# Kernel optimization log

Measured on AMD Instinct MI355X. Metric: run time of the kernel, lower is better.

Reference implementation:

```python
import jax, jax.numpy as jnp
import numpy as np
from jax import lax

C_LIGHT = 3e8
SPATIAL, CROP = 64, 128
BIN_LEN, WALL, SAMP_COEFF, CYCLES = 0.01, 2.0, 2.0, 5
B, D = 2, 1


def _waveconvparam(bin_resolution, virtual_wavelength, cycles):
    samples = int(round(cycles * virtual_wavelength / (C_LIGHT * bin_resolution)))
    num_cycles = samples * (C_LIGHT * bin_resolution) / virtual_wavelength
    sigma = 0.3
    g = np.arange(samples, dtype=np.float64)
    env = np.exp(-(((g - samples / 2.0) / (samples / 2.0)) ** 2) / (2 * sigma ** 2))
    cos_k = np.cos(2 * np.pi * num_cycles * g / samples) * env
    sin_k = np.sin(2 * np.pi * num_cycles * g / samples) * env
    return cos_k, sin_k


def _define_psf(N, M, slope):
    # LCT psf: locus of min |(4 slope)^2 (x^2+y^2) - z|, normalized and circularly shifted
    x = np.arange(2 * N, dtype=np.float64) / (2 * N - 1) * 2 - 1
    z = np.arange(2 * M, dtype=np.float64) / (2 * M - 1) * 2
    gy, gx, gz = np.meshgrid(x, x, z)  # (2N,2N,2M)
    blur = np.abs((4 * slope) ** 2 * (gx ** 2 + gy ** 2) - gz)
    d = (np.abs(blur - blur.min(axis=2, keepdims=True)) < 1e-8).astype(np.float64)
    e = d / np.sqrt(d.sum())
    f = np.roll(np.roll(e, N, axis=0), N, axis=1)
    return np.transpose(f, (2, 0, 1))  # (2M,2N,2N)


def _resampling_operator(M):
    row = M * M
    x = np.arange(1, row + 1, dtype=np.float64)
    mtx = np.zeros((row, M), dtype=np.float64)
    mtx[np.arange(row), np.ceil(np.sqrt(x)).astype(np.int64) - 1] = 1.0
    mtx = mtx / np.sqrt(x)[:, None]
    mtxi = mtx.T.copy()
    for _ in range(int(np.log2(M))):
        mtx = 0.5 * (mtx[0::2] + mtx[1::2])
        mtxi = 0.5 * (mtxi[:, 0::2] + mtxi[:, 1::2])
    return mtx.astype(np.float32), mtxi.astype(np.float32)


def setup_inputs() -> dict:
    key = jax.random.key(0)
    kf, kw, kb = jax.random.split(key, 3)
    bin_res = BIN_LEN / C_LIGHT
    trange = CROP * C_LIGHT * bin_res
    slope = (WALL / 2.0) / trange
    vlam = SAMP_COEFF * 2.0 * (WALL / (SPATIAL - 1))
    cos_k, sin_k = _waveconvparam(bin_res, vlam, CYCLES)
    wave = np.stack([cos_k, sin_k], 0)[:, ::-1][:, None, :].astype(np.float32)  # (2,1,k)
    psf = _define_psf(SPATIAL, CROP, slope)
    invpsf = np.conj(np.fft.fftn(psf))
    mtx, mtxi = _resampling_operator(CROP)
    return {
        "feature": jax.random.normal(kf, (B, D, CROP, SPATIAL, SPATIAL), jnp.float32),
        "conv_w": jax.random.normal(kw, ()) * 0.1 + 1.0,
        "conv_b": jax.random.normal(kb, ()) * 0.1,
        "wave": jnp.asarray(wave),
        "invpsf_real": jnp.asarray(np.real(invpsf).astype(np.float32))[None],
        "invpsf_imag": jnp.asarray(np.imag(invpsf).astype(np.float32))[None],
        "mtx": jnp.asarray(mtx),
        "mtxi": jnp.asarray(mtxi),
    }


def _attention(k1, k2, w, b):
    # SE-style cross attention; Conv3d(1,1,1) on unbatched (C=1,T,H,W) is w*x+b
    T = k2.shape[1]
    pe = jnp.sin(jnp.arange(T, dtype=k2.dtype))  # PE3D with 1 channel -> sin along T
    k2p = k2 + pe[None, :, None, None]
    scal = jnp.mean(w * k1 + b)  # conv + adaptive_avg_pool3d(1), channel dim = 1
    q = (w * k2p + b).reshape(1, 1, -1)
    attn = jax.nn.sigmoid(jax.nn.softmax(scal * q, axis=2)).reshape(k2p.shape)
    return attn * k2p


def _fre_atten2(kernel, w, b):
    _, T, H, W = kernel.shape
    ct, ch, cw = T // 2, H // 2, W // 2
    st, sh, sw = (T - ct) // 2, (H - ch) // 2, (W - cw) // 2
    sl = (slice(None), slice(ct - st, ct + st), slice(ch - sh, ch + sh), slice(cw - sw, cw + sw))
    high = kernel[sl]
    low = jnp.roll(kernel, (ct, ch, cw), axis=(1, 2, 3))[sl]
    l2l = _attention(low, low, w, b)
    l2h = _attention(l2l, high, w, b)
    temp = kernel.at[sl].set(l2h)
    temp = jnp.roll(temp, (ct, ch, cw), axis=(1, 2, 3)).at[sl].set(l2l)
    return jnp.roll(temp, (ct, ch, cw), axis=(1, 2, 3))


def _forward(feature, conv_w, conv_b, wave, invpsf_real, invpsf_imag, mtx, mtxi):
    b, d, T, H, W = feature.shape
    BD = b * d
    k = wave.shape[2]
    # virtual wave conv along time: (BDHW,1,T) x (2,1,k)
    data = feature.reshape(BD, T, H, W).transpose(0, 2, 3, 1).reshape(-1, 1, T)
    conv = lax.conv_general_dilated(data, wave, (1,), [(k // 2, k // 2)],
                                    dimension_numbers=("NCH", "OIH", "NCH"))
    if k % 2 == 0:
        conv = conv[:, :, 1:]
    data2 = conv.reshape(BD, H, W, 2, T).transpose(3, 0, 4, 1, 2).reshape(2 * BD, T, H, W)
    # temporal resampling then zero-pad to 2T,2H,2W
    tmp = jnp.einsum("tm,bmx->btx", mtx, data2.reshape(2 * BD, T, H * W)).reshape(2 * BD, T, H, W)
    datapad = jnp.zeros((2 * BD, 2 * T, 2 * H, 2 * W), feature.dtype).at[:, :T, :H, :W].set(tmp)
    datafre = jnp.fft.fftn(datapad)  # torch.fft.fftn transforms ALL dims incl. batch
    w1 = _fre_atten2(invpsf_real, conv_w, conv_b)
    w2 = _fre_atten2(invpsf_imag, conv_w, conv_b)
    re_real = datafre.real * w1 - datafre.imag * w2
    re_imag = datafre.real * w2 + datafre.imag * w1
    re = jnp.fft.ifftn(lax.complex(re_real, re_imag))
    vol = re[:, :T, :H, :W]
    cr, ci = vol[:BD].real, vol[:BD].imag
    sr, si = vol[BD:].real, vol[BD:].imag
    sum_real = cr ** 2 - ci ** 2 + sr ** 2 - si ** 2
    sum_imag = 2 * cr * ci + 2 * sr * si
    mag = jax.nn.relu((jnp.sqrt(sum_real ** 2 + sum_imag ** 2) + sum_real) * 0.5)
    sq = jnp.sqrt(mag)
    out = jnp.einsum("tm,bmx->btx", mtxi, sq.reshape(BD, T, H * W))
    return out.reshape(b, d, T, H, W)


def reference(feature, conv_w, conv_b, wave, invpsf_real, invpsf_imag, mtx, mtxi):
    return _forward(feature, conv_w, conv_b, wave, invpsf_real, invpsf_imag, mtx, mtxi)
```

## Files before the change

### kernel.cpp

```cpp
#include <hip/hip_runtime.h>

#define BLKE 524288
#define VOLE 4194304
#define TCROP 2097152
#define PI2 6.283185307179586476925286766559

__device__ __forceinline__ float2 cmulf(float2 a, float2 b){
  return make_float2(a.x*b.x - a.y*b.y, a.x*b.y + a.y*b.x);
}
__device__ __forceinline__ float waveSum(float v){
  #pragma unroll
  for (int o=32;o;o>>=1) v += __shfl_xor(v,o);
  return v;
}
__device__ __forceinline__ float waveMaxf(float v){
  #pragma unroll
  for (int o=32;o;o>>=1) v = fmaxf(v,__shfl_xor(v,o));
  return v;
}
__device__ __forceinline__ float waveMinf(float v){
  #pragma unroll
  for (int o=32;o;o>>=1) v = fminf(v,__shfl_xor(v,o));
  return v;
}

__device__ __forceinline__ void bcastReduce5(const float* __restrict__ pA, int kap,
    float& sum, float& mnl, float& mxl, float& mnh, float& mxh, float* sm ){
  int tid = threadIdx.x;
  const float* q = pA + kap*1280 + tid*5;
  float s = q[0], a = q[1], b = q[2], c = q[3], d = q[4];
  s = waveSum(s); a = waveMinf(a); b = waveMaxf(b); c = waveMinf(c); d = waveMaxf(d);
  if ((tid&63)==0){ int w = tid>>6; sm[w]=s; sm[4+w]=a; sm[8+w]=b; sm[12+w]=c; sm[16+w]=d; }
  __syncthreads();
  sum = sm[0]+sm[1]+sm[2]+sm[3];
  mnl = fminf(fminf(sm[4],sm[5]),fminf(sm[6],sm[7]));
  mxl = fmaxf(fmaxf(sm[8],sm[9]),fmaxf(sm[10],sm[11]));
  mnh = fminf(fminf(sm[12],sm[13]),fminf(sm[14],sm[15]));
  mxh = fmaxf(fmaxf(sm[16],sm[17]),fmaxf(sm[18],sm[19]));
}

__device__ __forceinline__ float bcastSum256(const float* __restrict__ p, float* sm ){
  int tid = threadIdx.x;
  float s = waveSum(p[tid]);
  if ((tid&63)==0) sm[tid>>6] = s;
  __syncthreads();
  return sm[0]+sm[1]+sm[2]+sm[3];
}

__global__ void kM(const float* __restrict__ mtx, const float* __restrict__ wave,
                   float* __restrict__ M){
  int idx = blockIdx.x*256 + threadIdx.x;
  int o = idx >> 14, r = idx & 16383;
  int t = r >> 7, s = r & 127;
  float acc = 0.f;
  int mlo = s-31; if (mlo < 0) mlo = 0;
  int mhi = s+31; if (mhi > 127) mhi = 127;
  for (int m = mlo; m <= mhi; m++) acc += mtx[t*128+m]*wave[o*63 + (s-m+31)];
  M[idx] = acc;
}

__global__ void __launch_bounds__(256) kTmp(const float* __restrict__ feat,
                                            const float* __restrict__ M,
                                            float* __restrict__ tmp){
  __shared__ float LF[32][64];
  __shared__ float LM[2][32][33];
  int b = blockIdx.z, tt = blockIdx.y, xt = blockIdx.x;
  int tid = threadIdx.x;
  int xx = tid & 63, tq = tid >> 6;
  float acc0[8] = {}, acc1[8] = {};
  const float* fb = feat + (size_t)b*BLKE;
  for (int sb = 0; sb < 4; sb++){
    #pragma unroll
    for (int j = 0; j < 8; j++){
      int idx = tid + j*256; int s = idx >> 6, x = idx & 63;
      LF[s][x] = fb[(size_t)(sb*32+s)*4096 + xt*64 + x];
    }
    #pragma unroll
    for (int j = 0; j < 8; j++){
      int idx = tid + j*256; int o = idx >> 10, r = idx & 1023;
      int trow = r >> 5, s = r & 31;
      LM[o][trow][s] = M[o*16384 + (tt*32+trow)*128 + sb*32+s];
    }
    __syncthreads();
    for (int s = 0; s < 32; s++){
      float f = LF[s][xx];
      #pragma unroll
      for (int i = 0; i < 8; i++){
        acc0[i] += LM[0][tq*8+i][s]*f;
        acc1[i] += LM[1][tq*8+i][s]*f;
      }
    }
    __syncthreads();
  }
  #pragma unroll
  for (int i = 0; i < 8; i++){
    int t = tt*32 + tq*8 + i;
    tmp[(size_t)(0*2+b)*BLKE + (size_t)t*4096 + xt*64+xx] = acc0[i];
    tmp[(size_t)(1*2+b)*BLKE + (size_t)t*4096 + xt*64+xx] = acc1[i];
  }
}

__global__ void __launch_bounds__(256) kRedA(const float* __restrict__ Kr,
                                             const float* __restrict__ Ki,
                                             float* __restrict__ Lw, float* __restrict__ Hw,
                                             float* __restrict__ pA){
  const float* K = blockIdx.y ? Ki : Kr;
  int kap = blockIdx.y;
  __shared__ float spe[128];
  __shared__ float sm[20];
  int tid = threadIdx.x;
  if (tid < 128) spe[tid] = sinf((float)tid);
  __syncthreads();
  float sum=0.f, mnl=3.4e38f, mxl=-3.4e38f, mnh=3.4e38f, mxh=-3.4e38f;
  int base = blockIdx.x*256 + tid;
  #pragma unroll
  for (int it = 0; it < 8; it++){
    int e = base + it*65536;
    int tau = e >> 12, rem = e & 4095, eta = rem >> 6, om = rem & 63;
    float pe = spe[tau];
    float lo = K[(size_t)((tau+192)&255)*16384 + ((eta+96)&127)*128 + ((om+96)&127)];
    float hi = K[(size_t)(tau+64)*16384 + (eta+32)*128 + (om+32)];
    sum += lo;
    float lp = lo+pe, hp = hi+pe;
    Lw[kap*BLKE + e] = lp;
    Hw[kap*BLKE + e] = hp;
    mnl=fminf(mnl,lp); mxl=fmaxf(mxl,lp);
    mnh=fminf(mnh,hp); mxh=fmaxf(mxh,hp);
  }
  sum = waveSum(sum); mnl=waveMinf(mnl); mxl=waveMaxf(mxl); mnh=waveMinf(mnh); mxh=waveMaxf(mxh);
  if ((tid&63)==0){ int w=tid>>6; sm[w]=sum; sm[4+w]=mnl; sm[8+w]=mxl; sm[12+w]=mnh; sm[16+w]=mxh; }
  __syncthreads();
  if (tid==0){
    float* o = pA + kap*1280 + blockIdx.x*5;
    o[0] = sm[0]+sm[1]+sm[2]+sm[3];
    o[1] = fminf(fminf(sm[4],sm[5]),fminf(sm[6],sm[7]));
    o[2] = fmaxf(fmaxf(sm[8],sm[9]),fmaxf(sm[10],sm[11]));
    o[3] = fminf(fminf(sm[12],sm[13]),fminf(sm[14],sm[15]));
    o[4] = fmaxf(fmaxf(sm[16],sm[17]),fmaxf(sm[18],sm[19]));
  }
}

__global__ void __launch_bounds__(256) kRedB(const float* __restrict__ pA,
                                             const float* __restrict__ Lw,
                                             float* __restrict__ pB,
                                             const float* cw, const float* cb){
  int kap = blockIdx.y;
  __shared__ float sm[20], smo[4];
  float sum,mnl,mxl,mnh,mxh;
  bcastReduce5(pA,kap,sum,mnl,mxl,mnh,mxh,sm);
  float w = cw[0], b = cb[0];
  float s1 = w*(sum*(1.0f/BLKE)) + b;
  float a1 = s1*w, c1 = s1*b;
  float mx = (a1>=0.f) ? a1*mxl+c1 : a1*mnl+c1;
  float acc = 0.f;
  int base = kap*BLKE + blockIdx.x*256 + threadIdx.x;
  #pragma unroll
  for (int it = 0; it < 8; it++){
    float lp = Lw[base + it*65536];
    acc += expf(a1*lp + c1 - mx);
  }
  acc = waveSum(acc);
  if ((threadIdx.x&63)==0) smo[threadIdx.x>>6] = acc;
  __syncthreads();
  if (threadIdx.x==0) pB[kap*256 + blockIdx.x] = smo[0]+smo[1]+smo[2]+smo[3];
}

__global__ void __launch_bounds__(256) kRedC(const float* __restrict__ pA,
                                             const float* __restrict__ pB,
                                             const float* __restrict__ Lw,
                                             float* __restrict__ pC,
                                             const float* cw, const float* cb){
  int kap = blockIdx.y;
  __shared__ float sm[20], smB[4], smo[4];
  float sum,mnl,mxl,mnh,mxh;
  bcastReduce5(pA,kap,sum,mnl,mxl,mnh,mxh,sm);
  float d1 = bcastSum256(pB + kap*256, smB);
  float w = cw[0], b = cb[0];
  float s1 = w*(sum*(1.0f/BLKE)) + b;
  float a1 = s1*w, c1 = s1*b;
  float mx = (a1>=0.f) ? a1*mxl+c1 : a1*mnl+c1;
  float invd = 1.0f/d1;
  float acc = 0.f;
  int base = kap*BLKE + blockIdx.x*256 + threadIdx.x;
  #pragma unroll
  for (int it = 0; it < 8; it++){
    float lp = Lw[base + it*65536];
    float p = expf(a1*lp + c1 - mx)*invd;
    acc += lp/(1.f + expf(-p));
  }
  acc = waveSum(acc);
  if ((threadIdx.x&63)==0) smo[threadIdx.x>>6] = acc;
  __syncthreads();
  if (threadIdx.x==0) pC[kap*256 + blockIdx.x] = smo[0]+smo[1]+smo[2]+smo[3];
}

__global__ void __launch_bounds__(256) kRedD(const float* __restrict__ pA,
                                             const float* __restrict__ pC,
                                             const float* __restrict__ Hw,
                                             float* __restrict__ pD,
                                             const float* cw, const float* cb){
  int kap = blockIdx.y;
  __shared__ float sm[20], smC[4], smo[4];
  float sum,mnl,mxl,mnh,mxh;
  bcastReduce5(pA,kap,sum,mnl,mxl,mnh,mxh,sm);
  float sl2 = bcastSum256(pC + kap*256, smC);
  float w = cw[0], b = cb[0];
  float s2 = w*(sl2*(1.0f/BLKE)) + b;
  float a2 = s2*w, c2 = s2*b;
  float mx = (a2>=0.f) ? a2*mxh+c2 : a2*mnh+c2;
  float acc = 0.f;
  int base = kap*BLKE + blockIdx.x*256 + threadIdx.x;
  #pragma unroll
  for (int it = 0; it < 8; it++){
    float hp = Hw[base + it*65536];
    acc += expf(a2*hp + c2 - mx);
  }
  acc = waveSum(acc);
  if ((threadIdx.x&63)==0) smo[threadIdx.x>>6] = acc;
  __syncthreads();
  if (threadIdx.x==0) pD[kap*256 + blockIdx.x] = smo[0]+smo[1]+smo[2]+smo[3];
}

__global__ void __launch_bounds__(256) kFin(const float* __restrict__ pA,
                                            const float* __restrict__ pB,
                                            const float* __restrict__ pC,
                                            const float* __restrict__ pD,
                                            float* __restrict__ scal,
                                            const float* cw, const float* cb){
  __shared__ float sm[20], smB[4], smC[4], smD[4];
  for (int kap = 0; kap < 2; kap++){
    if (kap) __syncthreads();
    float sum,mnl,mxl,mnh,mxh;
    bcastReduce5(pA,kap,sum,mnl,mxl,mnh,mxh,sm);
    float d1  = bcastSum256(pB + kap*256, smB);
    float sl2 = bcastSum256(pC + kap*256, smC);
    float d2  = bcastSum256(pD + kap*256, smD);
    if (threadIdx.x==0){
      float w = cw[0], b = cb[0];
      float s1 = w*(sum*(1.0f/BLKE)) + b;
      float a1 = s1*w, c1 = s1*b;
      float mx1 = (a1>=0.f) ? a1*mxl+c1 : a1*mnl+c1;
      float s2 = w*(sl2*(1.0f/BLKE)) + b;
      float a2 = s2*w, c2 = s2*b;
      float mx2 = (a2>=0.f) ? a2*mxh+c2 : a2*mnh+c2;
      float* Q = scal + kap*8;
      Q[0]=a1; Q[1]=c1; Q[2]=mx1; Q[3]=1.0f/d1;
      Q[4]=a2; Q[5]=c2; Q[6]=mx2; Q[7]=1.0f/d2;
    }
  }
}

__device__ __forceinline__ float attnv(float v, float a, float c, float mx, float invd){
  float p = expf(a*v + c - mx)*invd;
  return v / (1.f + expf(-p));
}
__device__ __forceinline__ float2 wcAt(int t, int h, int w,
                                       const float* __restrict__ Kr, const float* __restrict__ Ki,
                                       const float* spe, const float* P){
  size_t off = (size_t)t*16384 + (size_t)h*128 + w;
  float kr = Kr[off], ki = Ki[off];
  bool center = (t>=64 && t<192) && (h>=32 && h<96) && (w>=32 && w<96);
  int tc = (t+64)&255, hc = (h+32)&127, wc = (w+32)&127;
  bool corner = (tc<128) && (hc<64) && (wc<64);
  float2 o;
  if (center){
    float pe = spe[t-64];
    o.x = attnv(kr+pe, P[4],  P[5],  P[6],  P[7]);
    o.y = attnv(ki+pe, P[12], P[13], P[14], P[15]);
  } else if (corner){
    float pe = spe[tc];
    o.x = attnv(kr+pe, P[0], P[1],  P[2],  P[3]);
    o.y = attnv(ki+pe, P[8], P[9],  P[10], P[11]);
  } else {
    o.x = kr; o.y = ki;
  }
  return o;
}

__global__ void __launch_bounds__(256) kWc(const float* __restrict__ Kr,
                                           const float* __restrict__ Ki,
                                           const float* __restrict__ scal,
                                           float2* __restrict__ Wc){
  __shared__ float spe[128];
  __shared__ float P[16];
  int tid = threadIdx.x;
  if (tid < 128) spe[tid] = sinf((float)tid);
  if (tid < 16) P[tid] = scal[tid];
  __syncthreads();
  int idx = blockIdx.x*256 + tid;
  int t = idx >> 14, r = idx & 16383, h = r >> 7, w = r & 127;
  Wc[idx] = wcAt(t, h, w, Kr, Ki, spe, P);
}

__global__ void __launch_bounds__(256) kF1(const float* __restrict__ tmp,
                                           float2* __restrict__ Z2){
  __shared__ float2 bA[4][130], bB[4][130], tw[64];
  int tid = threadIdx.x;
  if (tid < 64){
    double ang = -PI2 * (double)tid / 128.0;
    tw[tid] = make_float2((float)cos(ang), (float)sin(ang));
  }
  int b = blockIdx.y;
  int l = tid >> 6, lane = tid & 63;
  int line = blockIdx.x*4 + l;
  int t = line >> 6, h = line & 63;
  const float* pc = tmp + (size_t)b*BLKE + (size_t)t*4096 + h*64;
  const float* ps = tmp + (size_t)(2+b)*BLKE + (size_t)t*4096 + h*64;
  bA[l][lane] = make_float2(pc[lane], ps[lane]);
  bA[l][lane+64] = make_float2(0.f, 0.f);
  __syncthreads();
  float2 (*src)[130] = bA, (*dst)[130] = bB;
  int m = 1;
  #pragma unroll
  for (int st = 0; st < 7; st++){
    int i = lane;
    int jm = i & ~(m-1);
    float2 a = src[l][i], b2 = src[l][i+64];
    float2 s = make_float2(a.x+b2.x, a.y+b2.y);
    float2 d = make_float2(a.x-b2.x, a.y-b2.y);
    dst[l][i+jm]   = s;
    dst[l][i+jm+m] = cmulf(d, tw[jm]);
    __syncthreads();
    float2 (*tp)[130] = src; src = dst; dst = tp;
    m <<= 1;
  }
  float2* outp = Z2 + (size_t)b*TCROP + (size_t)t*16384 + (size_t)h*128;
  outp[lane]    = src[l][lane];
  outp[lane+64] = src[l][lane+64];
}

__global__ void __launch_bounds__(256) kHf(float2* __restrict__ Z2){
  __shared__ float2 bA[16][130], bB[16][130], tw[64];
  int tid = threadIdx.x;
  if (tid < 64){
    double ang = -PI2 * (double)tid / 128.0;
    tw[tid] = make_float2((float)cos(ang), (float)sin(ang));
  }
  float2* Z = Z2 + (size_t)blockIdx.y*TCROP;
  int bid = blockIdx.x;
  int t = bid >> 3; int w0 = (bid & 7) << 4;
  size_t base = (size_t)t*16384 + w0;
  #pragma unroll
  for (int q = 0; q < 4; q++){
    int idx = q*256 + tid; int wl = idx & 15, hh = idx >> 4;
    bA[wl][hh] = Z[base + (size_t)hh*128 + wl];
    bA[wl][hh+64] = make_float2(0.f, 0.f);
  }
  __syncthreads();
  float2 (*src)[130] = bA, (*dst)[130] = bB;
  int m = 1;
  #pragma unroll
  for (int st = 0; st < 7; st++){
    #pragma unroll
    for (int q = 0; q < 4; q++){
      int g = q*256 + tid; int li = g >> 6; int i = g & 63;
      int jm = i & ~(m-1);
      float2 a = src[li][i], b2 = src[li][i+64];
      float2 s = make_float2(a.x+b2.x, a.y+b2.y);
      float2 d = make_float2(a.x-b2.x, a.y-b2.y);
      dst[li][i+jm]   = s;
      dst[li][i+jm+m] = cmulf(d, tw[jm]);
    }
    __syncthreads();
    float2 (*tp)[130] = src; src = dst; dst = tp;
    m <<= 1;
  }
  #pragma unroll
  for (int q = 0; q < 8; q++){
    int idx = q*256 + tid; int wl = idx & 15, hh = idx >> 4;
    Z[base + (size_t)hh*128 + wl] = src[wl][hh];
  }
}

__global__ void __launch_bounds__(256) kTfused(const float2* __restrict__ Z2,
                                               float2* __restrict__ U2,
                                               float2* __restrict__ V2,
                                               const float2* __restrict__ Wc){
  __shared__ float2 buf[16][259];
  __shared__ float2 tw[256];
  int tid = threadIdx.x;
  {
    double ang = -PI2 * (double)tid / 256.0;
    tw[tid] = make_float2((float)cos(ang), (float)sin(ang));
  }
  int b = blockIdx.y;
  int bid = blockIdx.x;
  int h = bid >> 3, w0 = (bid & 7) << 4;
  int wl = tid & 15, pq = tid >> 4;
  const float2* Z = Z2 + (size_t)b*TCROP;
  size_t gbase = (size_t)h*128 + w0 + wl;
  #pragma unroll
  for (int q = 0; q < 8; q++){
    int p = q*16 + pq;
    buf[wl][p] = Z[(size_t)p*16384 + gbase];
    buf[wl][p+128] = make_float2(0.f, 0.f);
  }
  __syncthreads();
  #pragma unroll
  for (int st = 0; st < 4; st++){
    const int Q = 64 >> (2*st);
    const int f = 1 << (2*st);
    #pragma unroll
    for (int it = 0; it < 4; it++){
      int u = pq + 16*it;
      int j = u & (Q-1);
      int seg = u >> (6 - 2*st);
      int base = (seg << (8 - 2*st)) + j;
      float2 a0 = buf[wl][base];
      float2 a1 = buf[wl][base+Q];
      float2 a2 = buf[wl][base+2*Q];
      float2 a3 = buf[wl][base+3*Q];
      float2 t0 = make_float2(a0.x+a2.x, a0.y+a2.y);
      float2 t1 = make_float2(a0.x-a2.x, a0.y-a2.y);
      float2 t2 = make_float2(a1.x+a3.x, a1.y+a3.y);
      float2 t3 = make_float2(a1.x-a3.x, a1.y-a3.y);
      float2 z0 = make_float2(t0.x+t2.x, t0.y+t2.y);
      float2 z2 = make_float2(t0.x-t2.x, t0.y-t2.y);
      float2 z1 = make_float2(t1.x+t3.y, t1.y-t3.x);
      float2 z3 = make_float2(t1.x-t3.y, t1.y+t3.x);
      buf[wl][base]     = z0;
      buf[wl][base+Q]   = cmulf(z1, tw[f*j]);
      buf[wl][base+2*Q] = cmulf(z2, tw[2*f*j]);
      buf[wl][base+3*Q] = cmulf(z3, tw[3*f*j]);
    }
    __syncthreads();
  }
  float2 rg[16];
  #pragma unroll
  for (int q = 0; q < 16; q++) rg[q] = buf[wl][q*16 + pq];
  #pragma unroll
  for (int q = 0; q < 16; q++){
    int p = q*16 + pq;
    int kt = ((p&3)<<6) | (((p>>2)&3)<<4) | (((p>>4)&3)<<2) | ((p>>6)&3);
    float2 wc = Wc[(size_t)kt*16384 + (size_t)h*128 + w0 + wl];
    buf[wl][p] = cmulf(rg[q], wc);
  }
  __syncthreads();
  #pragma unroll
  for (int st = 0; st < 4; st++){
    const int Q = 1 << (2*st);
    const int f = 64 >> (2*st);
    #pragma unroll
    for (int it = 0; it < 4; it++){
      int u = pq + 16*it;
      int j = u & (Q-1);
      int seg = u >> (2*st);
      int base = (seg << (2*st + 2)) + j;
      float2 w1 = tw[f*j], w2 = tw[2*f*j], w3 = tw[3*f*j];
      float2 a0 = buf[wl][base];
      float2 r1 = buf[wl][base+Q];
      float2 r2 = buf[wl][base+2*Q];
      float2 r3 = buf[wl][base+3*Q];
      float2 b1 = make_float2(r1.x*w1.x + r1.y*w1.y, r1.y*w1.x - r1.x*w1.y);
      float2 b2 = make_float2(r2.x*w2.x + r2.y*w2.y, r2.y*w2.x - r2.x*w2.y);
      float2 b3 = make_float2(r3.x*w3.x + r3.y*w3.y, r3.y*w3.x - r3.x*w3.y);
      float2 t0 = make_float2(a0.x+b2.x, a0.y+b2.y);
      float2 t1 = make_float2(a0.x-b2.x, a0.y-b2.y);
      float2 t2 = make_float2(b1.x+b3.x, b1.y+b3.y);
      float2 t3 = make_float2(b1.x-b3.x, b1.y-b3.y);
      buf[wl][base]     = make_float2(t0.x+t2.x, t0.y+t2.y);
      buf[wl][base+Q]   = make_float2(t1.x-t3.y, t1.y+t3.x);
      buf[wl][base+2*Q] = make_float2(t0.x-t2.x, t0.y-t2.y);
      buf[wl][base+3*Q] = make_float2(t1.x+t3.y, t1.y-t3.x);
    }
    __syncthreads();
  }
  float2* Uo = U2 + (size_t)b*TCROP;
  #pragma unroll
  for (int q = 0; q < 8; q++){
    int p = q*16 + pq;
    Uo[(size_t)p*16384 + gbase] = buf[wl][p];
  }
  #pragma unroll
  for (int q = 0; q < 16; q++){
    int p = q*16 + pq;
    int kt = ((p&3)<<6) | (((p>>2)&3)<<4) | (((p>>4)&3)<<2) | ((p>>6)&3);
    int tm = (256-kt)&255, hm = (128-h)&127, wm = (128-(w0+wl))&127;
    float2 wc = Wc[(size_t)tm*16384 + (size_t)hm*128 + wm];
    wc.y = -wc.y;
    buf[wl][p] = cmulf(rg[q], wc);
  }
  __syncthreads();
  #pragma unroll
  for (int st = 0; st < 4; st++){
    const int Q = 1 << (2*st);
    const int f = 64 >> (2*st);
    #pragma unroll
    for (int it = 0; it < 4; it++){
      int u = pq + 16*it;
      int j = u & (Q-1);
      int seg = u >> (2*st);
      int base = (seg << (2*st + 2)) + j;
      float2 w1 = tw[f*j], w2 = tw[2*f*j], w3 = tw[3*f*j];
      float2 a0 = buf[wl][base];
      float2 r1 = buf[wl][base+Q];
      float2 r2 = buf[wl][base+2*Q];
      float2 r3 = buf[wl][base+3*Q];
      float2 b1 = make_float2(r1.x*w1.x + r1.y*w1.y, r1.y*w1.x - r1.x*w1.y);
      float2 b2 = make_float2(r2.x*w2.x + r2.y*w2.y, r2.y*w2.x - r2.x*w2.y);
      float2 b3 = make_float2(r3.x*w3.x + r3.y*w3.y, r3.y*w3.x - r3.x*w3.y);
      float2 t0 = make_float2(a0.x+b2.x, a0.y+b2.y);
      float2 t1 = make_float2(a0.x-b2.x, a0.y-b2.y);
      float2 t2 = make_float2(b1.x+b3.x, b1.y+b3.y);
      float2 t3 = make_float2(b1.x-b3.x, b1.y-b3.y);
      buf[wl][base]     = make_float2(t0.x+t2.x, t0.y+t2.y);
      buf[wl][base+Q]   = make_float2(t1.x-t3.y, t1.y+t3.x);
      buf[wl][base+2*Q] = make_float2(t0.x-t2.x, t0.y-t2.y);
      buf[wl][base+3*Q] = make_float2(t1.x+t3.y, t1.y-t3.x);
    }
    __syncthreads();
  }
  float2* Vo = V2 + (size_t)b*TCROP;
  #pragma unroll
  for (int q = 0; q < 8; q++){
    int p = q*16 + pq;
    Vo[(size_t)p*16384 + gbase] = buf[wl][p];
  }
}

__global__ void __launch_bounds__(256) kHi(float2* __restrict__ U2, float2* __restrict__ V2){
  __shared__ float2 bA[16][130], bB[16][130], tw[64];
  int tid = threadIdx.x;
  if (tid < 64){
    double ang = PI2 * (double)tid / 128.0;
    tw[tid] = make_float2((float)cos(ang), (float)sin(ang));
  }
  float2* Z = (blockIdx.z ? V2 : U2) + (size_t)blockIdx.y*TCROP;
  int bid = blockIdx.x;
  int t = bid >> 3; int w0 = (bid & 7) << 4;
  size_t base = (size_t)t*16384 + w0;
  #pragma unroll
  for (int q = 0; q < 8; q++){
    int idx = q*256 + tid; int wl = idx & 15, hh = idx >> 4;
    bA[wl][hh] = Z[base + (size_t)hh*128 + wl];
  }
  __syncthreads();
  float2 (*src)[130] = bA, (*dst)[130] = bB;
  int m = 1;
  #pragma unroll
  for (int st = 0; st < 7; st++){
    #pragma unroll
    for (int q = 0; q < 4; q++){
      int g = q*256 + tid; int li = g >> 6; int i = g & 63;
      int jm = i & ~(m-1);
      float2 a = src[li][i], b2 = src[li][i+64];
      float2 s = make_float2(a.x+b2.x, a.y+b2.y);
      float2 d = make_float2(a.x-b2.x, a.y-b2.y);
      dst[li][i+jm]   = s;
      dst[li][i+jm+m] = cmulf(d, tw[jm]);
    }
    __syncthreads();
    float2 (*tp)[130] = src; src = dst; dst = tp;
    m <<= 1;
  }
  #pragma unroll
  for (int q = 0; q < 4; q++){
    int idx = q*256 + tid; int wl = idx & 15, hh = idx >> 4;
    Z[base + (size_t)hh*128 + wl] = src[wl][hh];
  }
}

__global__ void __launch_bounds__(256) kI3C(const float2* __restrict__ U2,
                                            const float2* __restrict__ V2,
                                            float* __restrict__ sq){
  __shared__ float2 bA[4][130], bB[4][130], tw[64];
  int tid = threadIdx.x;
  if (tid < 64){
    double ang = PI2 * (double)tid / 128.0;
    tw[tid] = make_float2((float)cos(ang), (float)sin(ang));
  }
  int b = blockIdx.y;
  int l = tid >> 6, lane = tid & 63;
  int line = blockIdx.x*4 + l;
  int t = line >> 6, h = line & 63;
  size_t off = (size_t)b*TCROP + (size_t)t*16384 + (size_t)h*128;
  bA[l][lane]    = U2[off + lane];
  bA[l][lane+64] = U2[off + lane + 64];
  __syncthreads();
  float2 (*src)[130] = bA, (*dst)[130] = bB;
  int m = 1;
  #pragma unroll
  for (int st = 0; st < 7; st++){
    int i = lane;
    int jm = i & ~(m-1);
    float2 a = src[l][i], b2 = src[l][i+64];
    float2 s = make_float2(a.x+b2.x, a.y+b2.y);
    float2 d = make_float2(a.x-b2.x, a.y-b2.y);
    dst[l][i+jm]   = s;
    dst[l][i+jm+m] = cmulf(d, tw[jm]);
    __syncthreads();
    float2 (*tp)[130] = src; src = dst; dst = tp;
    m <<= 1;
  }
  float2 y = src[l][lane];
  dst[l][lane]    = V2[off + lane];
  dst[l][lane+64] = V2[off + lane + 64];
  __syncthreads();
  src = dst; dst = (src == bA) ? bB : bA;
  m = 1;
  #pragma unroll
  for (int st = 0; st < 7; st++){
    int i = lane;
    int jm = i & ~(m-1);
    float2 a = src[l][i], b2 = src[l][i+64];
    float2 s = make_float2(a.x+b2.x, a.y+b2.y);
    float2 d = make_float2(a.x-b2.x, a.y-b2.y);
    dst[l][i+jm]   = s;
    dst[l][i+jm+m] = cmulf(d, tw[jm]);
    __syncthreads();
    float2 (*tp)[130] = src; src = dst; dst = tp;
    m <<= 1;
  }
  float2 v = src[l][lane];
  const float sc = 1.0f/(float)VOLE;
  const float sc2 = sc*sc;
  float2 s = cmulf(y, make_float2(v.x, -v.y));
  s.x *= sc2; s.y *= sc2;
  float mag = 0.5f*(sqrtf(s.x*s.x + s.y*s.y) + s.x);
  mag = fmaxf(mag, 0.f);
  sq[(size_t)b*BLKE + (size_t)t*4096 + h*64 + lane] = sqrtf(mag);
}

__global__ void __launch_bounds__(256) kOut(const float* __restrict__ sq,
                                            const float* __restrict__ mtxi,
                                            float* __restrict__ out){
  __shared__ float LF[32][64];
  __shared__ float LM[32][33];
  int b = blockIdx.z, tt = blockIdx.y, xt = blockIdx.x;
  int tid = threadIdx.x;
  int xx = tid & 63, tq = tid >> 6;
  float acc[8] = {};
  const float* fb = sq + (size_t)b*BLKE;
  for (int sb = 0; sb < 4; sb++){
    #pragma unroll
    for (int j = 0; j < 8; j++){
      int idx = tid + j*256; int s = idx >> 6, x = idx & 63;
      LF[s][x] = fb[(size_t)(sb*32+s)*4096 + xt*64 + x];
    }
    #pragma unroll
    for (int j = 0; j < 4; j++){
      int idx = tid + j*256; int trow = idx >> 5, s = idx & 31;
      LM[trow][s] = mtxi[(tt*32+trow)*128 + sb*32+s];
    }
    __syncthreads();
    for (int s = 0; s < 32; s++){
      float f = LF[s][xx];
      #pragma unroll
      for (int i = 0; i < 8; i++) acc[i] += LM[tq*8+i][s]*f;
    }
    __syncthreads();
  }
  #pragma unroll
  for (int i = 0; i < 8; i++){
    int t = tt*32 + tq*8 + i;
    out[(size_t)b*BLKE + (size_t)t*4096 + xt*64+xx] = acc[i];
  }
}

extern "C" void kernel_launch(void* const* d_in, const int* in_sizes, int n_in,
                              void* d_out, int out_size, void* d_ws, size_t ws_size,
                              hipStream_t stream){
  const float* feature = (const float*)d_in[0];
  const float* convW   = (const float*)d_in[1];
  const float* convB   = (const float*)d_in[2];
  const float* wave    = (const float*)d_in[3];
  const float* Kr      = (const float*)d_in[4];
  const float* Ki      = (const float*)d_in[5];
  const float* mtx     = (const float*)d_in[6];
  const float* mtxi    = (const float*)d_in[7];
  float* out = (float*)d_out;
  float* ws  = (float*)d_ws;

  float*  M    = ws;
  float*  scal = ws + 32768;
  float*  pA   = ws + 32832;
  float*  pB   = ws + 35392;
  float*  pC   = ws + 35904;
  float*  pD   = ws + 36416;
  float*  tmp  = ws + 65536;
  float*  sq   = ws + 65536 + 2097152;
  float2* Z2   = (float2*)(ws + 3211264);
  float2* U2   = (float2*)(ws + 11599872);
  float2* V2   = (float2*)(ws + 19988480);
  float2* Wc   = (float2*)(ws + 28377088);
  float*  Lw   = (float*)U2;
  float*  Hw   = ((float*)U2) + 1048576;

  kM<<<128, 256, 0, stream>>>(mtx, wave, M);
  kTmp<<<dim3(64,4,2), 256, 0, stream>>>(feature, M, tmp);
  kRedA<<<dim3(256,2), 256, 0, stream>>>(Kr, Ki, Lw, Hw, pA);
  kRedB<<<dim3(256,2), 256, 0, stream>>>(pA, Lw, pB, convW, convB);
  kRedC<<<dim3(256,2), 256, 0, stream>>>(pA, pB, Lw, pC, convW, convB);
  kRedD<<<dim3(256,2), 256, 0, stream>>>(pA, pC, Hw, pD, convW, convB);
  kFin<<<1, 256, 0, stream>>>(pA, pB, pC, pD, scal, convW, convB);
  kWc<<<16384, 256, 0, stream>>>(Kr, Ki, scal, Wc);

  kF1<<<dim3(2048,2), 256, 0, stream>>>(tmp, Z2);
  kHf<<<dim3(1024,2), 256, 0, stream>>>(Z2);
  kTfused<<<dim3(1024,2), 256, 0, stream>>>(Z2, U2, V2, Wc);
  kHi<<<dim3(1024,2,2), 256, 0, stream>>>(U2, V2);
  kI3C<<<dim3(2048,2), 256, 0, stream>>>(U2, V2, sq);
  kOut<<<dim3(64,4,2), 256, 0, stream>>>(sq, mtxi, out);
}
```

Baseline: 286.4 us.

## Co-schedule independent reduction and FFT stages in merged kernels by block ranges

Measured after the change: 273.6 us, median of 2. -4.5%, faster.

```diff
diff --git a/kernel.cpp b/kernel.cpp
--- a/kernel.cpp
+++ b/kernel.cpp
@@ -47,205 +47,275 @@
   return sm[0]+sm[1]+sm[2]+sm[3];
 }
 
-__global__ void kM(const float* __restrict__ mtx, const float* __restrict__ wave,
-                   float* __restrict__ M){
-  int idx = blockIdx.x*256 + threadIdx.x;
-  int o = idx >> 14, r = idx & 16383;
-  int t = r >> 7, s = r & 127;
-  float acc = 0.f;
-  int mlo = s-31; if (mlo < 0) mlo = 0;
-  int mhi = s+31; if (mhi > 127) mhi = 127;
-  for (int m = mlo; m <= mhi; m++) acc += mtx[t*128+m]*wave[o*63 + (s-m+31)];
-  M[idx] = acc;
-}
-
-__global__ void __launch_bounds__(256) kTmp(const float* __restrict__ feat,
-                                            const float* __restrict__ M,
-                                            float* __restrict__ tmp){
-  __shared__ float LF[32][64];
-  __shared__ float LM[2][32][33];
-  int b = blockIdx.z, tt = blockIdx.y, xt = blockIdx.x;
-  int tid = threadIdx.x;
-  int xx = tid & 63, tq = tid >> 6;
-  float acc0[8] = {}, acc1[8] = {};
-  const float* fb = feat + (size_t)b*BLKE;
-  for (int sb = 0; sb < 4; sb++){
-    #pragma unroll
-    for (int j = 0; j < 8; j++){
-      int idx = tid + j*256; int s = idx >> 6, x = idx & 63;
-      LF[s][x] = fb[(size_t)(sb*32+s)*4096 + xt*64 + x];
-    }
-    #pragma unroll
-    for (int j = 0; j < 8; j++){
-      int idx = tid + j*256; int o = idx >> 10, r = idx & 1023;
-      int trow = r >> 5, s = r & 31;
-      LM[o][trow][s] = M[o*16384 + (tt*32+trow)*128 + sb*32+s];
-    }
-    __syncthreads();
-    for (int s = 0; s < 32; s++){
-      float f = LF[s][xx];
-      #pragma unroll
-      for (int i = 0; i < 8; i++){
-        acc0[i] += LM[0][tq*8+i][s]*f;
-        acc1[i] += LM[1][tq*8+i][s]*f;
-      }
-    }
-    __syncthreads();
-  }
-  #pragma unroll
-  for (int i = 0; i < 8; i++){
-    int t = tt*32 + tq*8 + i;
-    tmp[(size_t)(0*2+b)*BLKE + (size_t)t*4096 + xt*64+xx] = acc0[i];
-    tmp[(size_t)(1*2+b)*BLKE + (size_t)t*4096 + xt*64+xx] = acc1[i];
-  }
-}
-
-__global__ void __launch_bounds__(256) kRedA(const float* __restrict__ Kr,
-                                             const float* __restrict__ Ki,
-                                             float* __restrict__ Lw, float* __restrict__ Hw,
-                                             float* __restrict__ pA){
-  const float* K = blockIdx.y ? Ki : Kr;
-  int kap = blockIdx.y;
+__global__ void __launch_bounds__(256) kD1(const float* __restrict__ mtx,
+                                           const float* __restrict__ wave,
+                                           float* __restrict__ M,
+                                           const float* __restrict__ Kr,
+                                           const float* __restrict__ Ki,
+                                           float* __restrict__ Lw, float* __restrict__ Hw,
+                                           float* __restrict__ pA){
   __shared__ float spe[128];
   __shared__ float sm[20];
-  int tid = threadIdx.x;
-  if (tid < 128) spe[tid] = sinf((float)tid);
-  __syncthreads();
-  float sum=0.f, mnl=3.4e38f, mxl=-3.4e38f, mnh=3.4e38f, mxh=-3.4e38f;
-  int base = blockIdx.x*256 + tid;
-  #pragma unroll
-  for (int it = 0; it < 8; it++){
-    int e = base + it*65536;
-    int tau = e >> 12, rem = e & 4095, eta = rem >> 6, om = rem & 63;
-    float pe = spe[tau];
-    float lo = K[(size_t)((tau+192)&255)*16384 + ((eta+96)&127)*128 + ((om+96)&127)];
-    float hi = K[(size_t)(tau+64)*16384 + (eta+32)*128 + (om+32)];
-    sum += lo;
-    float lp = lo+pe, hp = hi+pe;
-    Lw[kap*BLKE + e] = lp;
-    Hw[kap*BLKE + e] = hp;
-    mnl=fminf(mnl,lp); mxl=fmaxf(mxl,lp);
-    mnh=fminf(mnh,hp); mxh=fmaxf(mxh,hp);
-  }
-  sum = waveSum(sum); mnl=waveMinf(mnl); mxl=waveMaxf(mxl); mnh=waveMinf(mnh); mxh=waveMaxf(mxh);
-  if ((tid&63)==0){ int w=tid>>6; sm[w]=sum; sm[4+w]=mnl; sm[8+w]=mxl; sm[12+w]=mnh; sm[16+w]=mxh; }
-  __syncthreads();
-  if (tid==0){
-    float* o = pA + kap*1280 + blockIdx.x*5;
-    o[0] = sm[0]+sm[1]+sm[2]+sm[3];
-    o[1] = fminf(fminf(sm[4],sm[5]),fminf(sm[6],sm[7]));
-    o[2] = fmaxf(fmaxf(sm[8],sm[9]),fmaxf(sm[10],sm[11]));
-    o[3] = fminf(fminf(sm[12],sm[13]),fminf(sm[14],sm[15]));
-    o[4] = fmaxf(fmaxf(sm[16],sm[17]),fmaxf(sm[18],sm[19]));
-  }
-}
-
-__global__ void __launch_bounds__(256) kRedB(const float* __restrict__ pA,
-                                             const float* __restrict__ Lw,
-                                             float* __restrict__ pB,
-                                             const float* cw, const float* cb){
-  int kap = blockIdx.y;
+  int bid = blockIdx.x;
+  int tid = threadIdx.x;
+  if (bid < 512){
+    int kap = bid >> 8, bx = bid & 255;
+    const float* K = kap ? Ki : Kr;
+    if (tid < 128) spe[tid] = sinf((float)tid);
+    __syncthreads();
+    float sum=0.f, mnl=3.4e38f, mxl=-3.4e38f, mnh=3.4e38f, mxh=-3.4e38f;
+    int base = bx*256 + tid;
+    #pragma unroll
+    for (int it = 0; it < 8; it++){
+      int e = base + it*65536;
+      int tau = e >> 12, rem = e & 4095, eta = rem >> 6, om = rem & 63;
+      float pe = spe[tau];
+      float lo = K[(size_t)((tau+192)&255)*16384 + ((eta+96)&127)*128 + ((om+96)&127)];
+      float hi = K[(size_t)(tau+64)*16384 + (eta+32)*128 + (om+32)];
+      sum += lo;
+      float lp = lo+pe, hp = hi+pe;
+      Lw[kap*BLKE + e] = lp;
+      Hw[kap*BLKE + e] = hp;
+      mnl=fminf(mnl,lp); mxl=fmaxf(mxl,lp);
+      mnh=fminf(mnh,hp); mxh=fmaxf(mxh,hp);
+    }
+    sum = waveSum(sum); mnl=waveMinf(mnl); mxl=waveMaxf(mxl); mnh=waveMinf(mnh); mxh=waveMaxf(mxh);
+    if ((tid&63)==0){ int w=tid>>6; sm[w]=sum; sm[4+w]=mnl; sm[8+w]=mxl; sm[12+w]=mnh; sm[16+w]=mxh; }
+    __syncthreads();
+    if (tid==0){
+      float* o = pA + kap*1280 + bx*5;
+      o[0] = sm[0]+sm[1]+sm[2]+sm[3];
+      o[1] = fminf(fminf(sm[4],sm[5]),fminf(sm[6],sm[7]));
+      o[2] = fmaxf(fmaxf(sm[8],sm[9]),fmaxf(sm[10],sm[11]));
+      o[3] = fminf(fminf(sm[12],sm[13]),fminf(sm[14],sm[15]));
+      o[4] = fmaxf(fmaxf(sm[16],sm[17]),fmaxf(sm[18],sm[19]));
+    }
+  } else {
+    int idx = (bid-512)*256 + tid;
+    int o = idx >> 14, r = idx & 16383;
+    int t = r >> 7, s = r & 127;
+    float acc = 0.f;
+    int mlo = s-31; if (mlo < 0) mlo = 0;
+    int mhi = s+31; if (mhi > 127) mhi = 127;
+    for (int m = mlo; m <= mhi; m++) acc += mtx[t*128+m]*wave[o*63 + (s-m+31)];
+    M[idx] = acc;
+  }
+}
+
+__global__ void __launch_bounds__(256) kD2(const float* __restrict__ feat,
+                                           const float* __restrict__ M,
+                                           float* __restrict__ tmp,
+                                           const float* __restrict__ pA,
+                                           const float* __restrict__ Lw,
+                                           float* __restrict__ pB,
+                                           const float* cw, const float* cb){
+  __shared__ __align__(16) char smem[16640];
   __shared__ float sm[20], smo[4];
-  float sum,mnl,mxl,mnh,mxh;
-  bcastReduce5(pA,kap,sum,mnl,mxl,mnh,mxh,sm);
-  float w = cw[0], b = cb[0];
-  float s1 = w*(sum*(1.0f/BLKE)) + b;
-  float a1 = s1*w, c1 = s1*b;
-  float mx = (a1>=0.f) ? a1*mxl+c1 : a1*mnl+c1;
-  float acc = 0.f;
-  int base = kap*BLKE + blockIdx.x*256 + threadIdx.x;
-  #pragma unroll
-  for (int it = 0; it < 8; it++){
-    float lp = Lw[base + it*65536];
-    acc += expf(a1*lp + c1 - mx);
-  }
-  acc = waveSum(acc);
-  if ((threadIdx.x&63)==0) smo[threadIdx.x>>6] = acc;
-  __syncthreads();
-  if (threadIdx.x==0) pB[kap*256 + blockIdx.x] = smo[0]+smo[1]+smo[2]+smo[3];
-}
-
-__global__ void __launch_bounds__(256) kRedC(const float* __restrict__ pA,
-                                             const float* __restrict__ pB,
-                                             const float* __restrict__ Lw,
-                                             float* __restrict__ pC,
-                                             const float* cw, const float* cb){
-  int kap = blockIdx.y;
-  __shared__ float sm[20], smB[4], smo[4];
-  float sum,mnl,mxl,mnh,mxh;
-  bcastReduce5(pA,kap,sum,mnl,mxl,mnh,mxh,sm);
-  float d1 = bcastSum256(pB + kap*256, smB);
-  float w = cw[0], b = cb[0];
-  float s1 = w*(sum*(1.0f/BLKE)) + b;
-  float a1 = s1*w, c1 = s1*b;
-  float mx = (a1>=0.f) ? a1*mxl+c1 : a1*mnl+c1;
-  float invd = 1.0f/d1;
-  float acc = 0.f;
-  int base = kap*BLKE + blockIdx.x*256 + threadIdx.x;
-  #pragma unroll
-  for (int it = 0; it < 8; it++){
-    float lp = Lw[base + it*65536];
-    float p = expf(a1*lp + c1 - mx)*invd;
-    acc += lp/(1.f + expf(-p));
-  }
-  acc = waveSum(acc);
-  if ((threadIdx.x&63)==0) smo[threadIdx.x>>6] = acc;
-  __syncthreads();
-  if (threadIdx.x==0) pC[kap*256 + blockIdx.x] = smo[0]+smo[1]+smo[2]+smo[3];
-}
-
-__global__ void __launch_bounds__(256) kRedD(const float* __restrict__ pA,
-                                             const float* __restrict__ pC,
-                                             const float* __restrict__ Hw,
-                                             float* __restrict__ pD,
-                                             const float* cw, const float* cb){
-  int kap = blockIdx.y;
-  __shared__ float sm[20], smC[4], smo[4];
-  float sum,mnl,mxl,mnh,mxh;
-  bcastReduce5(pA,kap,sum,mnl,mxl,mnh,mxh,sm);
-  float sl2 = bcastSum256(pC + kap*256, smC);
-  float w = cw[0], b = cb[0];
-  float s2 = w*(sl2*(1.0f/BLKE)) + b;
-  float a2 = s2*w, c2 = s2*b;
-  float mx = (a2>=0.f) ? a2*mxh+c2 : a2*mnh+c2;
-  float acc = 0.f;
-  int base = kap*BLKE + blockIdx.x*256 + threadIdx.x;
-  #pragma unroll
-  for (int it = 0; it < 8; it++){
-    float hp = Hw[base + it*65536];
-    acc += expf(a2*hp + c2 - mx);
-  }
-  acc = waveSum(acc);
-  if ((threadIdx.x&63)==0) smo[threadIdx.x>>6] = acc;
-  __syncthreads();
-  if (threadIdx.x==0) pD[kap*256 + blockIdx.x] = smo[0]+smo[1]+smo[2]+smo[3];
-}
-
-__global__ void __launch_bounds__(256) kFin(const float* __restrict__ pA,
-                                            const float* __restrict__ pB,
-                                            const float* __restrict__ pC,
-                                            const float* __restrict__ pD,
-                                            float* __restrict__ scal,
-                                            const float* cw, const float* cb){
-  __shared__ float sm[20], smB[4], smC[4], smD[4];
-  for (int kap = 0; kap < 2; kap++){
-    if (kap) __syncthreads();
+  int bid = blockIdx.x;
+  int tid = threadIdx.x;
+  if (bid < 512){
+    int kap = bid >> 8, bx = bid & 255;
     float sum,mnl,mxl,mnh,mxh;
     bcastReduce5(pA,kap,sum,mnl,mxl,mnh,mxh,sm);
-    float d1  = bcastSum256(pB + kap*256, smB);
+    float w = cw[0], b = cb[0];
+    float s1 = w*(sum*(1.0f/BLKE)) + b;
+    float a1 = s1*w, c1 = s1*b;
+    float mx = (a1>=0.f) ? a1*mxl+c1 : a1*mnl+c1;
+    float acc = 0.f;
+    int base = kap*BLKE + bx*256 + tid;
+    #pragma unroll
+    for (int it = 0; it < 8; it++){
+      float lp = Lw[base + it*65536];
+      acc += expf(a1*lp + c1 - mx);
+    }
+    acc = waveSum(acc);
+    if ((tid&63)==0) smo[tid>>6] = acc;
+    __syncthreads();
+    if (tid==0) pB[kap*256 + bx] = smo[0]+smo[1]+smo[2]+smo[3];
+  } else {
+    int e = bid - 512;
+    int b = e >> 8, tt = (e >> 6) & 3, xt = e & 63;
+    float (*LF)[64] = (float(*)[64])smem;
+    float (*LM)[32][33] = (float(*)[32][33])(smem + 8192);
+    int xx = tid & 63, tq = tid >> 6;
+    float acc0[8] = {}, acc1[8] = {};
+    const float* fb = feat + (size_t)b*BLKE;
+    for (int sb = 0; sb < 4; sb++){
+      #pragma unroll
+      for (int j = 0; j < 8; j++){
+        int idx = tid + j*256; int s = idx >> 6, x = idx & 63;
+        LF[s][x] = fb[(size_t)(sb*32+s)*4096 + xt*64 + x];
+      }
+      #pragma unroll
+      for (int j = 0; j < 8; j++){
+        int idx = tid + j*256; int o = idx >> 10, r = idx & 1023;
+        int trow = r >> 5, s = r & 31;
+        LM[o][trow][s] = M[o*16384 + (tt*32+trow)*128 + sb*32+s];
+      }
+      __syncthreads();
+      for (int s = 0; s < 32; s++){
+        float f = LF[s][xx];
+        #pragma unroll
+        for (int i = 0; i < 8; i++){
+          acc0[i] += LM[0][tq*8+i][s]*f;
+          acc1[i] += LM[1][tq*8+i][s]*f;
+        }
+      }
+      __syncthreads();
+    }
+    #pragma unroll
+    for (int i = 0; i < 8; i++){
+      int t = tt*32 + tq*8 + i;
+      tmp[(size_t)(0*2+b)*BLKE + (size_t)t*4096 + xt*64+xx] = acc0[i];
+      tmp[(size_t)(1*2+b)*BLKE + (size_t)t*4096 + xt*64+xx] = acc1[i];
+    }
+  }
+}
+
+__global__ void __launch_bounds__(256) kD3(const float* __restrict__ tmp,
+                                           float2* __restrict__ Z2,
+                                           const float* __restrict__ pA,
+                                           const float* __restrict__ pB,
+                                           const float* __restrict__ Lw,
+                                           float* __restrict__ pC,
+                                           const float* cw, const float* cb){
+  __shared__ __align__(16) char smem[8832];
+  __shared__ float sm[20], smB[4], smo[4];
+  int bid = blockIdx.x;
+  int tid = threadIdx.x;
+  if (bid < 512){
+    int kap = bid >> 8, bx = bid & 255;
+    float sum,mnl,mxl,mnh,mxh;
+    bcastReduce5(pA,kap,sum,mnl,mxl,mnh,mxh,sm);
+    float d1 = bcastSum256(pB + kap*256, smB);
+    float w = cw[0], b = cb[0];
+    float s1 = w*(sum*(1.0f/BLKE)) + b;
+    float a1 = s1*w, c1 = s1*b;
+    float mx = (a1>=0.f) ? a1*mxl+c1 : a1*mnl+c1;
+    float invd = 1.0f/d1;
+    float acc = 0.f;
+    int base = kap*BLKE + bx*256 + tid;
+    #pragma unroll
+    for (int it = 0; it < 8; it++){
+      float lp = Lw[base + it*65536];
+      float p = expf(a1*lp + c1 - mx)*invd;
+      acc += lp/(1.f + expf(-p));
+    }
+    acc = waveSum(acc);
+    if ((tid&63)==0) smo[tid>>6] = acc;
+    __syncthreads();
+    if (tid==0) pC[kap*256 + bx] = smo[0]+smo[1]+smo[2]+smo[3];
+  } else {
+    int e = bid - 512;
+    int b = e >> 11, bx = e & 2047;
+    float2 (*bA)[130] = (float2(*)[130])smem;
+    float2 (*bB)[130] = (float2(*)[130])(smem + 4160);
+    float2* tw = (float2*)(smem + 8320);
+    if (tid < 64){
+      double ang = -PI2 * (double)tid / 128.0;
+      tw[tid] = make_float2((float)cos(ang), (float)sin(ang));
+    }
+    int l = tid >> 6, lane = tid & 63;
+    int line = bx*4 + l;
+    int t = line >> 6, h = line & 63;
+    const float* pc = tmp + (size_t)b*BLKE + (size_t)t*4096 + h*64;
+    const float* ps = tmp + (size_t)(2+b)*BLKE + (size_t)t*4096 + h*64;
+    bA[l][lane] = make_float2(pc[lane], ps[lane]);
+    bA[l][lane+64] = make_float2(0.f, 0.f);
+    __syncthreads();
+    float2 (*src)[130] = bA, (*dst)[130] = bB;
+    int m = 1;
+    #pragma unroll
+    for (int st = 0; st < 7; st++){
+      int i = lane;
+      int jm = i & ~(m-1);
+      float2 a = src[l][i], b2 = src[l][i+64];
+      float2 s = make_float2(a.x+b2.x, a.y+b2.y);
+      float2 d = make_float2(a.x-b2.x, a.y-b2.y);
+      dst[l][i+jm]   = s;
+      dst[l][i+jm+m] = cmulf(d, tw[jm]);
+      __syncthreads();
+      float2 (*tp)[130] = src; src = dst; dst = tp;
+      m <<= 1;
+    }
+    float2* outp = Z2 + (size_t)b*TCROP + (size_t)t*16384 + (size_t)h*128;
+    outp[lane]    = src[l][lane];
+    outp[lane+64] = src[l][lane+64];
+  }
+}
+
+__global__ void __launch_bounds__(256) kD4(float2* __restrict__ Z2,
+                                           const float* __restrict__ pA,
+                                           const float* __restrict__ pC,
+                                           const float* __restrict__ Hw,
+                                           float* __restrict__ pD,
+                                           const float* cw, const float* cb){
+  __shared__ __align__(16) char smem[33792];
+  __shared__ float sm[20], smC[4], smo[4];
+  int bid = blockIdx.x;
+  int tid = threadIdx.x;
+  if (bid < 512){
+    int kap = bid >> 8, bx = bid & 255;
+    float sum,mnl,mxl,mnh,mxh;
+    bcastReduce5(pA,kap,sum,mnl,mxl,mnh,mxh,sm);
     float sl2 = bcastSum256(pC + kap*256, smC);
-    float d2  = bcastSum256(pD + kap*256, smD);
-    if (threadIdx.x==0){
-      float w = cw[0], b = cb[0];
-      float s1 = w*(sum*(1.0f/BLKE)) + b;
-      float a1 = s1*w, c1 = s1*b;
-      float mx1 = (a1>=0.f) ? a1*mxl+c1 : a1*mnl+c1;
-      float s2 = w*(sl2*(1.0f/BLKE)) + b;
-      float a2 = s2*w, c2 = s2*b;
-      float mx2 = (a2>=0.f) ? a2*mxh+c2 : a2*mnh+c2;
-      float* Q = scal + kap*8;
-      Q[0]=a1; Q[1]=c1; Q[2]=mx1; Q[3]=1.0f/d1;
-      Q[4]=a2; Q[5]=c2; Q[6]=mx2; Q[7]=1.0f/d2;
+    float w = cw[0], b = cb[0];
+    float s2 = w*(sl2*(1.0f/BLKE)) + b;
+    float a2 = s2*w, c2 = s2*b;
+    float mx = (a2>=0.f) ? a2*mxh+c2 : a2*mnh+c2;
+    float acc = 0.f;
+    int base = kap*BLKE + bx*256 + tid;
+    #pragma unroll
+    for (int it = 0; it < 8; it++){
+      float hp = Hw[base + it*65536];
+      acc += expf(a2*hp + c2 - mx);
+    }
+    acc = waveSum(acc);
+    if ((tid&63)==0) smo[tid>>6] = acc;
+    __syncthreads();
+    if (tid==0) pD[kap*256 + bx] = smo[0]+smo[1]+smo[2]+smo[3];
+  } else {
+    int e = bid - 512;
+    int b = e >> 10, bx = e & 1023;
+    float2 (*bA)[130] = (float2(*)[130])smem;
+    float2 (*bB)[130] = (float2(*)[130])(smem + 16640);
+    float2* tw = (float2*)(smem + 33280);
+    if (tid < 64){
+      double ang = -PI2 * (double)tid / 128.0;
+      tw[tid] = make_float2((float)cos(ang), (float)sin(ang));
+    }
+    float2* Z = Z2 + (size_t)b*TCROP;
+    int t = bx >> 3; int w0 = (bx & 7) << 4;
+    size_t base = (size_t)t*16384 + w0;
+    #pragma unroll
+    for (int q = 0; q < 4; q++){
+      int idx = q*256 + tid; int wl = idx & 15, hh = idx >> 4;
+      bA[wl][hh] = Z[base + (size_t)hh*128 + wl];
+      bA[wl][hh+64] = make_float2(0.f, 0.f);
+    }
+    __syncthreads();
+    float2 (*src)[130] = bA, (*dst)[130] = bB;
+    int m = 1;
+    #pragma unroll
+    for (int st = 0; st < 7; st++){
+      #pragma unroll
+      for (int q = 0; q < 4; q++){
+        int g = q*256 + tid; int li = g >> 6; int i = g & 63;
+        int jm = i & ~(m-1);
+        float2 a = src[li][i], b2 = src[li][i+64];
+        float2 s = make_float2(a.x+b2.x, a.y+b2.y);
+        float2 d = make_float2(a.x-b2.x, a.y-b2.y);
+        dst[li][i+jm]   = s;
+        dst[li][i+jm+m] = cmulf(d, tw[jm]);
+      }
+      __syncthreads();
+      float2 (*tp)[130] = src; src = dst; dst = tp;
+      m <<= 1;
+    }
+    #pragma unroll
+    for (int q = 0; q < 8; q++){
+      int idx = q*256 + tid; int wl = idx & 15, hh = idx >> 4;
+      Z[base + (size_t)hh*128 + wl] = src[wl][hh];
     }
   }
 }
@@ -277,98 +347,45 @@
   return o;
 }
 
-__global__ void __launch_bounds__(256) kWc(const float* __restrict__ Kr,
-                                           const float* __restrict__ Ki,
-                                           const float* __restrict__ scal,
-                                           float2* __restrict__ Wc){
+__global__ void __launch_bounds__(256) kWcF(const float* __restrict__ Kr,
+                                            const float* __restrict__ Ki,
+                                            const float* __restrict__ pA,
+                                            const float* __restrict__ pB,
+                                            const float* __restrict__ pC,
+                                            const float* __restrict__ pD,
+                                            const float* cw, const float* cb,
+                                            float2* __restrict__ Wc){
   __shared__ float spe[128];
   __shared__ float P[16];
+  __shared__ float sm[20], smB[4], smC[4], smD[4];
   int tid = threadIdx.x;
   if (tid < 128) spe[tid] = sinf((float)tid);
-  if (tid < 16) P[tid] = scal[tid];
-  __syncthreads();
-  int idx = blockIdx.x*256 + tid;
-  int t = idx >> 14, r = idx & 16383, h = r >> 7, w = r & 127;
-  Wc[idx] = wcAt(t, h, w, Kr, Ki, spe, P);
-}
-
-__global__ void __launch_bounds__(256) kF1(const float* __restrict__ tmp,
-                                           float2* __restrict__ Z2){
-  __shared__ float2 bA[4][130], bB[4][130], tw[64];
-  int tid = threadIdx.x;
-  if (tid < 64){
-    double ang = -PI2 * (double)tid / 128.0;
-    tw[tid] = make_float2((float)cos(ang), (float)sin(ang));
-  }
-  int b = blockIdx.y;
-  int l = tid >> 6, lane = tid & 63;
-  int line = blockIdx.x*4 + l;
-  int t = line >> 6, h = line & 63;
-  const float* pc = tmp + (size_t)b*BLKE + (size_t)t*4096 + h*64;
-  const float* ps = tmp + (size_t)(2+b)*BLKE + (size_t)t*4096 + h*64;
-  bA[l][lane] = make_float2(pc[lane], ps[lane]);
-  bA[l][lane+64] = make_float2(0.f, 0.f);
-  __syncthreads();
-  float2 (*src)[130] = bA, (*dst)[130] = bB;
-  int m = 1;
-  #pragma unroll
-  for (int st = 0; st < 7; st++){
-    int i = lane;
-    int jm = i & ~(m-1);
-    float2 a = src[l][i], b2 = src[l][i+64];
-    float2 s = make_float2(a.x+b2.x, a.y+b2.y);
-    float2 d = make_float2(a.x-b2.x, a.y-b2.y);
-    dst[l][i+jm]   = s;
-    dst[l][i+jm+m] = cmulf(d, tw[jm]);
-    __syncthreads();
-    float2 (*tp)[130] = src; src = dst; dst = tp;
-    m <<= 1;
-  }
-  float2* outp = Z2 + (size_t)b*TCROP + (size_t)t*16384 + (size_t)h*128;
-  outp[lane]    = src[l][lane];
-  outp[lane+64] = src[l][lane+64];
-}
-
-__global__ void __launch_bounds__(256) kHf(float2* __restrict__ Z2){
-  __shared__ float2 bA[16][130], bB[16][130], tw[64];
-  int tid = threadIdx.x;
-  if (tid < 64){
-    double ang = -PI2 * (double)tid / 128.0;
-    tw[tid] = make_float2((float)cos(ang), (float)sin(ang));
-  }
-  float2* Z = Z2 + (size_t)blockIdx.y*TCROP;
-  int bid = blockIdx.x;
-  int t = bid >> 3; int w0 = (bid & 7) << 4;
-  size_t base = (size_t)t*16384 + w0;
+  for (int kap = 0; kap < 2; kap++){
+    if (kap) __syncthreads();
+    float sum,mnl,mxl,mnh,mxh;
+    bcastReduce5(pA,kap,sum,mnl,mxl,mnh,mxh,sm);
+    float d1  = bcastSum256(pB + kap*256, smB);
+    float sl2 = bcastSum256(pC + kap*256, smC);
+    float d2  = bcastSum256(pD + kap*256, smD);
+    if (tid==0){
+      float w = cw[0], b = cb[0];
+      float s1 = w*(sum*(1.0f/BLKE)) + b;
+      float a1 = s1*w, c1 = s1*b;
+      float mx1 = (a1>=0.f) ? a1*mxl+c1 : a1*mnl+c1;
+      float s2 = w*(sl2*(1.0f/BLKE)) + b;
+      float a2 = s2*w, c2 = s2*b;
+      float mx2 = (a2>=0.f) ? a2*mxh+c2 : a2*mnh+c2;
+      float* Q = P + kap*8;
+      Q[0]=a1; Q[1]=c1; Q[2]=mx1; Q[3]=1.0f/d1;
+      Q[4]=a2; Q[5]=c2; Q[6]=mx2; Q[7]=1.0f/d2;
+    }
+  }
+  __syncthreads();
   #pragma unroll
   for (int q = 0; q < 4; q++){
-    int idx = q*256 + tid; int wl = idx & 15, hh = idx >> 4;
-    bA[wl][hh] = Z[base + (size_t)hh*128 + wl];
-    bA[wl][hh+64] = make_float2(0.f, 0.f);
-  }
-  __syncthreads();
-  float2 (*src)[130] = bA, (*dst)[130] = bB;
-  int m = 1;
-  #pragma unroll
-  for (int st = 0; st < 7; st++){
-    #pragma unroll
-    for (int q = 0; q < 4; q++){
-      int g = q*256 + tid; int li = g >> 6; int i = g & 63;
-      int jm = i & ~(m-1);
-      float2 a = src[li][i], b2 = src[li][i+64];
-      float2 s = make_float2(a.x+b2.x, a.y+b2.y);
-      float2 d = make_float2(a.x-b2.x, a.y-b2.y);
-      dst[li][i+jm]   = s;
-      dst[li][i+jm+m] = cmulf(d, tw[jm]);
-    }
-    __syncthreads();
-    float2 (*tp)[130] = src; src = dst; dst = tp;
-    m <<= 1;
-  }
-  #pragma unroll
-  for (int q = 0; q < 8; q++){
-    int idx = q*256 + tid; int wl = idx & 15, hh = idx >> 4;
-    Z[base + (size_t)hh*128 + wl] = src[wl][hh];
+    int idx = blockIdx.x*1024 + q*256 + tid;
+    int t = idx >> 14, r = idx & 16383, h = r >> 7, w = r & 127;
+    Wc[idx] = wcAt(t, h, w, Kr, Ki, spe, P);
   }
 }
 
@@ -672,7 +689,6 @@
   float* ws  = (float*)d_ws;
 
   float*  M    = ws;
-  float*  scal = ws + 32768;
   float*  pA   = ws + 32832;
   float*  pB   = ws + 35392;
   float*  pC   = ws + 35904;
@@ -686,17 +702,11 @@
   float*  Lw   = (float*)U2;
   float*  Hw   = ((float*)U2) + 1048576;
 
-  kM<<<128, 256, 0, stream>>>(mtx, wave, M);
-  kTmp<<<dim3(64,4,2), 256, 0, stream>>>(feature, M, tmp);
-  kRedA<<<dim3(256,2), 256, 0, stream>>>(Kr, Ki, Lw, Hw, pA);
-  kRedB<<<dim3(256,2), 256, 0, stream>>>(pA, Lw, pB, convW, convB);
-  kRedC<<<dim3(256,2), 256, 0, stream>>>(pA, pB, Lw, pC, convW, convB);
-  kRedD<<<dim3(256,2), 256, 0, stream>>>(pA, pC, Hw, pD, convW, convB);
-  kFin<<<1, 256, 0, stream>>>(pA, pB, pC, pD, scal, convW, convB);
-  kWc<<<16384, 256, 0, stream>>>(Kr, Ki, scal, Wc);
-
-  kF1<<<dim3(2048,2), 256, 0, stream>>>(tmp, Z2);
-  kHf<<<dim3(1024,2), 256, 0, stream>>>(Z2);
+  kD1 <<<640,  256, 0, stream>>>(mtx, wave, M, Kr, Ki, Lw, Hw, pA);
+  kD2 <<<1024, 256, 0, stream>>>(feature, M, tmp, pA, Lw, pB, convW, convB);
+  kD3 <<<4608, 256, 0, stream>>>(tmp, Z2, pA, pB, Lw, pC, convW, convB);
+  kD4 <<<2560, 256, 0, stream>>>(Z2, pA, pC, Hw, pD, convW, convB);
+  kWcF<<<4096, 256, 0, stream>>>(Kr, Ki, pA, pB, pC, pD, convW, convB, Wc);
   kTfused<<<dim3(1024,2), 256, 0, stream>>>(Z2, U2, V2, Wc);
   kHi<<<dim3(1024,2,2), 256, 0, stream>>>(U2, V2);
   kI3C<<<dim3(2048,2), 256, 0, stream>>>(U2, V2, sq);
```
